# Optimization experiments

Measured on AMD Instinct MI355X. Metric: run time of the kernel, lower is better.

The kernel has to match this reference:

```python
import jax, jax.numpy as jnp
import numpy as np

B, T, D, H, L, V = 32, 128, 384, 6, 6, 32000
HS = D // H  # 64, head_size
EPS = 1e-5   # nn.LayerNorm default


def setup_inputs() -> dict:
    key = jax.random.key(0)
    ks = jax.random.split(key, 12)
    n = lambda k, shp: jax.random.normal(k, shp, dtype=jnp.float32) * 0.02
    return {
        'tokens': jax.random.randint(ks[0], (B, T), 0, V, dtype=jnp.int32),
        'tok_emb': n(ks[1], (V, D)),
        'pos_emb': n(ks[2], (T, D)),
        'Wq': n(ks[3], (L, H, D, HS)),
        'Wk': n(ks[4], (L, H, D, HS)),
        'Wv': n(ks[5], (L, H, D, HS)),
        'Wo': n(ks[6], (L, D, D)),
        'bo': jnp.zeros((L, D), jnp.float32),
        'W1': n(ks[7], (L, D, 4 * D)),
        'b1': jnp.zeros((L, 4 * D), jnp.float32),
        'W2': n(ks[8], (L, 4 * D, D)),
        'b2': jnp.zeros((L, D), jnp.float32),
        'g1': jnp.ones((L, D), jnp.float32),
        'be1': jnp.zeros((L, D), jnp.float32),
        'g2': jnp.ones((L, D), jnp.float32),
        'be2': jnp.zeros((L, D), jnp.float32),
        'gf': jnp.ones((D,), jnp.float32),
        'bef': jnp.zeros((D,), jnp.float32),
        'Wout': n(ks[9], (D, V)),
        'bout': jnp.zeros((V,), jnp.float32),
    }


def _ln(x, g, b):
    m = x.mean(-1, keepdims=True)
    v = ((x - m) ** 2).mean(-1, keepdims=True)
    return (x - m) * jax.lax.rsqrt(v + EPS) * g + b


def reference(tokens, tok_emb, pos_emb, Wq, Wk, Wv, Wo, bo, W1, b1, W2, b2,
              g1, be1, g2, be2, gf, bef, Wout, bout):
    t = tokens.shape[1]
    x = tok_emb[tokens] + pos_emb[:t]  # [B,T,D]
    mask = jnp.tril(jnp.ones((t, t), dtype=bool))
    scale = HS ** -0.5

    def block(x, p):
        wq, wk, wv, wo, bo_, w1, b1_, w2, b2_, g1_, be1_, g2_, be2_ = p
        h = _ln(x, g1_, be1_)
        q = jnp.einsum('btd,hde->bhte', h, wq)
        k = jnp.einsum('btd,hde->bhte', h, wk)
        v = jnp.einsum('btd,hde->bhte', h, wv)
        s = jnp.einsum('bhqe,bhke->bhqk', q, k) * scale
        s = jnp.where(mask, s, -jnp.inf)
        a = jax.nn.softmax(s, axis=-1)
        o = jnp.einsum('bhqk,bhke->bhqe', a, v)  # [B,H,T,HS]
        o = o.transpose(0, 2, 1, 3).reshape(x.shape[0], t, D)
        x = x + o @ wo + bo_
        h2 = _ln(x, g2_, be2_)
        x = x + jax.nn.relu(h2 @ w1 + b1_) @ w2 + b2_
        return x, None

    x, _ = jax.lax.scan(block, x, (Wq, Wk, Wv, Wo, bo, W1, b1, W2, b2,
                                   g1, be1, g2, be2))
    x = _ln(x, gf, bef)
    logits = x @ Wout + bout  # [B,T,V]
    return jax.nn.softmax(logits, axis=-1)
```

## Files before the change

kernel.cpp:

```cpp
#include <hip/hip_runtime.h>
#include <math.h>

#define NB 32
#define NT 128
#define ND 384
#define NH 6
#define NL 6
#define NV 32000
#define NHS 64
#define NBT (NB*NT)
#define NFF (4*ND)
#define NQKV (3*ND)
#define LNEPS 1e-5f

typedef unsigned short u16;
typedef unsigned int   u32;
typedef __attribute__((ext_vector_type(8))) short bf16x8;
typedef __attribute__((ext_vector_type(4))) float f32x4;

#define FLAG_BIAS 1
#define FLAG_RELU 2
#define FLAG_RESID 4
#define FLAG_BF16OUT 8

__device__ __forceinline__ float bf2f(u16 h) { return __uint_as_float((u32)h << 16); }
__device__ __forceinline__ u16 f2bf(float f) {
    u32 u = __float_as_uint(f);
    u32 r = u + 0x7fffu + ((u >> 16) & 1u);
    return (u16)(r >> 16);
}

__device__ __forceinline__ float wave_sum(float v) {
#pragma unroll
    for (int m = 1; m < 64; m <<= 1) v += __shfl_xor(v, m, 64);
    return v;
}
__device__ __forceinline__ float wave_max(float v) {
#pragma unroll
    for (int m = 1; m < 64; m <<= 1) v = fmaxf(v, __shfl_xor(v, m, 64));
    return v;
}

__global__ void embed_kernel(const int* __restrict__ tokens,
                             const float* __restrict__ te,
                             const float* __restrict__ pe,
                             float* __restrict__ x) {
    int i = blockIdx.x * 256 + threadIdx.x;
    if (i >= NBT * ND) return;
    int d  = i % ND;
    int bt = i / ND;
    int t  = bt % NT;
    int tok = tokens[bt];
    x[i] = te[(size_t)tok * ND + d] + pe[t * ND + d];
}

__global__ __launch_bounds__(256) void transpose_cvt_kernel(
    const float* __restrict__ in, u16* __restrict__ out,
    int R, int C, long in_z_stride, long out_z_stride, int zH, long out_h_stride)
{
    __shared__ float tile[32][33];
    int z = blockIdx.z;
    long in_off = (long)z * in_z_stride;
    long out_off;
    if (zH > 1) { int l = z / zH, h = z % zH;
        out_off = (long)l * out_z_stride + (long)h * out_h_stride; }
    else out_off = (long)z * out_z_stride;
    int r0 = blockIdx.y * 32, c0 = blockIdx.x * 32;
    int tx = threadIdx.x & 31, ty = threadIdx.x >> 5;
#pragma unroll
    for (int i = 0; i < 32; i += 8)
        tile[ty + i][tx] = in[in_off + (size_t)(r0 + ty + i) * C + c0 + tx];
    __syncthreads();
#pragma unroll
    for (int i = 0; i < 32; i += 8)
        out[out_off + (size_t)(c0 + ty + i) * R + r0 + tx] = f2bf(tile[tx][ty + i]);
}

template <int BF16OUT>
__global__ __launch_bounds__(256) void ln_kernel(const float* __restrict__ x,
                                                 const float* __restrict__ g,
                                                 const float* __restrict__ be,
                                                 float* __restrict__ outf,
                                                 u16* __restrict__ outb) {
    __shared__ float red[4];
    int row = blockIdx.x, tid = threadIdx.x;
    const float* xr = x + (size_t)row * ND;
    float v0 = xr[tid];
    bool has1 = (tid + 256) < ND;
    float v1 = has1 ? xr[tid + 256] : 0.f;

    float s = wave_sum(v0 + v1);
    if ((tid & 63) == 0) red[tid >> 6] = s;
    __syncthreads();
    float mean = (red[0] + red[1] + red[2] + red[3]) * (1.f / ND);
    __syncthreads();

    float d0 = v0 - mean;
    float d1 = has1 ? (v1 - mean) : 0.f;
    float ss = wave_sum(d0 * d0 + d1 * d1);
    if ((tid & 63) == 0) red[tid >> 6] = ss;
    __syncthreads();
    float rstd = rsqrtf((red[0] + red[1] + red[2] + red[3]) * (1.f / ND) + LNEPS);

    float o0 = d0 * rstd * g[tid] + be[tid];
    if (BF16OUT) {
        u16* orow = outb + (size_t)row * ND;
        orow[tid] = f2bf(o0);
        if (has1) orow[tid + 256] = f2bf(d1 * rstd * g[tid + 256] + be[tid + 256]);
    } else {
        float* orow = outf + (size_t)row * ND;
        orow[tid] = o0;
        if (has1) orow[tid + 256] = d1 * rstd * g[tid + 256] + be[tid + 256];
    }
}

#define BM 128
#define BN 128
#define BK 32
#define KPAD 40

__global__ __launch_bounds__(256) void gemm_bf16_kernel(
    const u16* __restrict__ A,
    const u16* __restrict__ Bt,
    const float* __restrict__ bias,
    float* __restrict__ Cf,
    u16* __restrict__ Cb,
    int M, int N, int K, int flags)
{
    __shared__ u16 As[BM * KPAD];
    __shared__ u16 Bs[BN * KPAD];
    int tid = threadIdx.x;
    int bn = blockIdx.x, bm = blockIdx.y;
    int row0 = bm * BM, col0 = bn * BN;
    int wave = tid >> 6, lane = tid & 63;
    int wr = wave >> 1, wc = wave & 1;
    int lrow = lane & 15;
    int kgrp = lane >> 4;

    f32x4 acc[4][4];
#pragma unroll
    for (int i = 0; i < 4; i++)
#pragma unroll
        for (int j = 0; j < 4; j++) acc[i][j] = (f32x4){0.f, 0.f, 0.f, 0.f};

    int c0 = tid * 2;
    int sr0 = c0 >> 2, sk0 = (c0 & 3) * 8;
    int c1 = c0 + 1;
    int sr1 = c1 >> 2, sk1 = (c1 & 3) * 8;

    const size_t arow0 = (size_t)(row0 + sr0) * K;
    const size_t arow1 = (size_t)(row0 + sr1) * K;
    const size_t brow0 = (size_t)(col0 + sr0) * K;
    const size_t brow1 = (size_t)(col0 + sr1) * K;

    for (int k0 = 0; k0 < K; k0 += BK) {
        bf16x8 a0 = *(const bf16x8*)&A[arow0 + k0 + sk0];
        bf16x8 a1 = *(const bf16x8*)&A[arow1 + k0 + sk1];
        bf16x8 b0 = *(const bf16x8*)&Bt[brow0 + k0 + sk0];
        bf16x8 b1 = *(const bf16x8*)&Bt[brow1 + k0 + sk1];
        __syncthreads();
        *(bf16x8*)&As[sr0 * KPAD + sk0] = a0;
        *(bf16x8*)&As[sr1 * KPAD + sk1] = a1;
        *(bf16x8*)&Bs[sr0 * KPAD + sk0] = b0;
        *(bf16x8*)&Bs[sr1 * KPAD + sk1] = b1;
        __syncthreads();

        bf16x8 af[4], bfr[4];
#pragma unroll
        for (int mi = 0; mi < 4; mi++)
            af[mi] = *(const bf16x8*)&As[(wr * 64 + mi * 16 + lrow) * KPAD + kgrp * 8];
#pragma unroll
        for (int ni = 0; ni < 4; ni++)
            bfr[ni] = *(const bf16x8*)&Bs[(wc * 64 + ni * 16 + lrow) * KPAD + kgrp * 8];
#pragma unroll
        for (int mi = 0; mi < 4; mi++)
#pragma unroll
            for (int ni = 0; ni < 4; ni++)
                acc[mi][ni] = __builtin_amdgcn_mfma_f32_16x16x32_bf16(
                    af[mi], bfr[ni], acc[mi][ni], 0, 0, 0);
    }

#pragma unroll
    for (int mi = 0; mi < 4; mi++) {
#pragma unroll
        for (int ni = 0; ni < 4; ni++) {
            int c = col0 + wc * 64 + ni * 16 + lrow;
            int rb = row0 + wr * 64 + mi * 16 + kgrp * 4;
#pragma unroll
            for (int j = 0; j < 4; j++) {
                size_t idx = (size_t)(rb + j) * N + c;
                float v = acc[mi][ni][j];
                if (flags & FLAG_BIAS) v += bias[c];
                if (flags & FLAG_RELU) v = fmaxf(v, 0.f);
                if (flags & FLAG_RESID) v += Cf[idx];
                if (flags & FLAG_BF16OUT) Cb[idx] = f2bf(v);
                else Cf[idx] = v;
            }
        }
    }
}

__global__ __launch_bounds__(256) void gemm_f32_kernel(const float* __restrict__ A,
                                                       const float* __restrict__ Bm,
                                                       const float* __restrict__ bias,
                                                       float* __restrict__ C,
                                                       int M, int N, int K, int flags) {
    __shared__ float Asl[16][65];
    __shared__ float Bsl[16][64];
    int bn = blockIdx.x, bm = blockIdx.y;
    int tid = threadIdx.x;
    int tr = tid >> 4, tc = tid & 15;
    int row0 = bm * 64, col0 = bn * 64;
    float acc[4][4];
#pragma unroll
    for (int i = 0; i < 4; i++)
#pragma unroll
        for (int j = 0; j < 4; j++) acc[i][j] = 0.f;

    for (int k0 = 0; k0 < K; k0 += 16) {
#pragma unroll
        for (int i = tid; i < 1024; i += 256) {
            int r = i >> 4, c = i & 15;
            Asl[c][r] = A[(size_t)(row0 + r) * K + (k0 + c)];
        }
#pragma unroll
        for (int i = tid; i < 1024; i += 256) {
            int r = i >> 6, c = i & 63;
            Bsl[r][c] = Bm[(size_t)(k0 + r) * N + (col0 + c)];
        }
        __syncthreads();
#pragma unroll
        for (int kk = 0; kk < 16; kk++) {
            float a[4], bv[4];
#pragma unroll
            for (int i = 0; i < 4; i++) a[i] = Asl[kk][tr * 4 + i];
#pragma unroll
            for (int j = 0; j < 4; j++) bv[j] = Bsl[kk][tc * 4 + j];
#pragma unroll
            for (int i = 0; i < 4; i++)
#pragma unroll
                for (int j = 0; j < 4; j++) acc[i][j] += a[i] * bv[j];
        }
        __syncthreads();
    }
#pragma unroll
    for (int i = 0; i < 4; i++) {
        size_t r = (size_t)row0 + tr * 4 + i;
#pragma unroll
        for (int j = 0; j < 4; j++) {
            int cc = col0 + tc * 4 + j;
            float t = acc[i][j];
            if (flags & 1) t += bias[cc];
            C[r * (size_t)N + cc] = t;
        }
    }
}

__global__ __launch_bounds__(128) void attn_kernel(const u16* __restrict__ qkv,
                                                   u16* __restrict__ o) {
    __shared__ float ks[NT][NHS];
    __shared__ float vs[NT][NHS];
    int bh = blockIdx.x;
    int b = bh / NH, h = bh % NH;
    int tid = threadIdx.x;
    size_t row0 = (size_t)b * NT;

    for (int i = tid; i < NT * (NHS / 8); i += 128) {
        int r = i >> 3, c8 = (i & 7) * 8;
        bf16x8 kv = *(const bf16x8*)&qkv[(row0 + r) * NQKV + ND + h * NHS + c8];
        bf16x8 vv = *(const bf16x8*)&qkv[(row0 + r) * NQKV + 2 * ND + h * NHS + c8];
#pragma unroll
        for (int j = 0; j < 8; j++) {
            ks[r][c8 + j] = bf2f((u16)kv[j]);
            vs[r][c8 + j] = bf2f((u16)vv[j]);
        }
    }
    float qr[NHS];
    {
        const u16* qp = &qkv[(row0 + tid) * NQKV + h * NHS];
#pragma unroll
        for (int e8 = 0; e8 < 8; e8++) {
            bf16x8 qv = *(const bf16x8*)(qp + e8 * 8);
#pragma unroll
            for (int j = 0; j < 8; j++) qr[e8 * 8 + j] = bf2f((u16)qv[j]);
        }
    }
    __syncthreads();

    const float scale = 0.125f;
    float m = -1e30f;
    for (int j = 0; j <= tid; ++j) {
        float dot = 0.f;
#pragma unroll
        for (int e = 0; e < NHS; e++) dot += qr[e] * ks[j][e];
        m = fmaxf(m, dot * scale);
    }
    float acc[NHS];
#pragma unroll
    for (int e = 0; e < NHS; e++) acc[e] = 0.f;
    float s = 0.f;
    for (int j = 0; j <= tid; ++j) {
        float dot = 0.f;
#pragma unroll
        for (int e = 0; e < NHS; e++) dot += qr[e] * ks[j][e];
        float p = __expf(dot * scale - m);
        s += p;
#pragma unroll
        for (int e = 0; e < NHS; e++) acc[e] += p * vs[j][e];
    }
    float inv = 1.f / s;
    u16* op = o + (row0 + tid) * ND + h * NHS;
#pragma unroll
    for (int e = 0; e < NHS; e++) op[e] = f2bf(acc[e] * inv);
}

__global__ __launch_bounds__(1024) void softmax_kernel(float* __restrict__ out) {
    __shared__ float red[16];
    int row = blockIdx.x, tid = threadIdx.x;
    float* p = out + (size_t)row * NV;
    const int nch = NV / 4;
    float4 v[8];
    float m = -1e30f;
#pragma unroll
    for (int i = 0; i < 8; i++) {
        int c = tid + i * 1024;
        if (c < nch) {
            v[i] = ((const float4*)p)[c];
            m = fmaxf(m, fmaxf(fmaxf(v[i].x, v[i].y), fmaxf(v[i].z, v[i].w)));
        }
    }
    m = wave_max(m);
    if ((tid & 63) == 0) red[tid >> 6] = m;
    __syncthreads();
    float mm = red[0];
#pragma unroll
    for (int i = 1; i < 16; i++) mm = fmaxf(mm, red[i]);
    __syncthreads();
    float s = 0.f;
#pragma unroll
    for (int i = 0; i < 8; i++) {
        int c = tid + i * 1024;
        if (c < nch) {
            v[i].x = __expf(v[i].x - mm); v[i].y = __expf(v[i].y - mm);
            v[i].z = __expf(v[i].z - mm); v[i].w = __expf(v[i].w - mm);
            s += v[i].x + v[i].y + v[i].z + v[i].w;
        }
    }
    s = wave_sum(s);
    if ((tid & 63) == 0) red[tid >> 6] = s;
    __syncthreads();
    float ss = 0.f;
#pragma unroll
    for (int i = 0; i < 16; i++) ss += red[i];
    float inv = 1.f / ss;
#pragma unroll
    for (int i = 0; i < 8; i++) {
        int c = tid + i * 1024;
        if (c < nch) {
            v[i].x *= inv; v[i].y *= inv; v[i].z *= inv; v[i].w *= inv;
            ((float4*)p)[c] = v[i];
        }
    }
}

extern "C" void kernel_launch(void* const* d_in, const int* in_sizes, int n_in,
                              void* d_out, int out_size, void* d_ws, size_t ws_size,
                              hipStream_t stream) {
    const int*   tokens  = (const int*)d_in[0];
    const float* tok_emb = (const float*)d_in[1];
    const float* pos_emb = (const float*)d_in[2];
    const float* Wq      = (const float*)d_in[3];
    const float* Wk      = (const float*)d_in[4];
    const float* Wv      = (const float*)d_in[5];
    const float* Wo      = (const float*)d_in[6];
    const float* bo      = (const float*)d_in[7];
    const float* W1      = (const float*)d_in[8];
    const float* b1      = (const float*)d_in[9];
    const float* W2      = (const float*)d_in[10];
    const float* b2      = (const float*)d_in[11];
    const float* g1      = (const float*)d_in[12];
    const float* be1     = (const float*)d_in[13];
    const float* g2      = (const float*)d_in[14];
    const float* be2     = (const float*)d_in[15];
    const float* gf      = (const float*)d_in[16];
    const float* bef     = (const float*)d_in[17];
    const float* Wout    = (const float*)d_in[18];
    const float* bout    = (const float*)d_in[19];
    float* out = (float*)d_out;

    const size_t S_hb   = (size_t)NBT * ND * 2;
    const size_t S_wout = (size_t)NV * ND * 2;
    const size_t S_x    = (size_t)NBT * ND * 4;
    const size_t S_qkv  = (size_t)NBT * NQKV * 2;
    const size_t S_o    = (size_t)NBT * ND * 2;
    const size_t S_u    = (size_t)NBT * NFF * 2;
    const size_t S_wqkv = (size_t)NL * NQKV * ND * 2;
    const size_t S_wo   = (size_t)NL * ND * ND * 2;
    const size_t S_w1   = (size_t)NL * ND * NFF * 2;
    const size_t S_w2   = (size_t)NL * NFF * ND * 2;
    const size_t S_hf   = (size_t)NBT * ND * 4;
    auto al = [](size_t x) { return (x + 255) & ~(size_t)255; };

    const size_t needA = al(S_hb) + al(S_wout) + al(S_x) + al(S_qkv) + al(S_o) +
                         al(S_u) + al(S_wqkv) + al(S_wo) + al(S_w1) + al(S_w2);
    const size_t needB = al(S_hb) + al(S_wout);

    char* wsb  = (char*)d_ws;
    char* outb = (char*)d_out;
    bool fp32_logits = false;

    u16 *hb, *woutt, *qkvb, *ob, *ub, *wqkvt, *wot, *w1t, *w2t;
    float *xbuf, *hf = nullptr;

    if (ws_size >= needA) {
        char* p = wsb;
        hb    = (u16*)p; p += al(S_hb);
        woutt = (u16*)p; p += al(S_wout);
        xbuf  = (float*)p; p += al(S_x);
        qkvb  = (u16*)p; p += al(S_qkv);
        ob    = (u16*)p; p += al(S_o);
        ub    = (u16*)p; p += al(S_u);
        wqkvt = (u16*)p; p += al(S_wqkv);
        wot   = (u16*)p; p += al(S_wo);
        w1t   = (u16*)p; p += al(S_w1);
        w2t   = (u16*)p; p += al(S_w2);
    } else if (ws_size >= needB) {
        char* p = wsb;
        hb    = (u16*)p; p += al(S_hb);
        woutt = (u16*)p; p += al(S_wout);
        char* q = outb;
        xbuf  = (float*)q; q += al(S_x);
        qkvb  = (u16*)q; q += al(S_qkv);
        ob    = (u16*)q; q += al(S_o);
        ub    = (u16*)q; q += al(S_u);
        wqkvt = (u16*)q; q += al(S_wqkv);
        wot   = (u16*)q; q += al(S_wo);
        w1t   = (u16*)q; q += al(S_w1);
        w2t   = (u16*)q; q += al(S_w2);
    } else {
        fp32_logits = true;
        hf = (float*)wsb;
        woutt = nullptr;
        char* q = outb;
        hb    = (u16*)q; q += al(S_hb);
        xbuf  = (float*)q; q += al(S_x);
        qkvb  = (u16*)q; q += al(S_qkv);
        ob    = (u16*)q; q += al(S_o);
        ub    = (u16*)q; q += al(S_u);
        wqkvt = (u16*)q; q += al(S_wqkv);
        wot   = (u16*)q; q += al(S_wo);
        w1t   = (u16*)q; q += al(S_w1);
        w2t   = (u16*)q; q += al(S_w2);
    }

    {
        const float* Wsides[3] = {Wq, Wk, Wv};
        for (int s = 0; s < 3; s++)
            transpose_cvt_kernel<<<dim3(NHS / 32, ND / 32, NL * NH), 256, 0, stream>>>(
                Wsides[s], wqkvt + (size_t)s * ND * ND, ND, NHS,
                (long)ND * NHS, (long)NQKV * ND, NH, (long)NHS * ND);
        transpose_cvt_kernel<<<dim3(ND / 32, ND / 32, NL), 256, 0, stream>>>(
            Wo, wot, ND, ND, (long)ND * ND, (long)ND * ND, 1, 0);
        transpose_cvt_kernel<<<dim3(NFF / 32, ND / 32, NL), 256, 0, stream>>>(
            W1, w1t, ND, NFF, (long)ND * NFF, (long)NFF * ND, 1, 0);
        transpose_cvt_kernel<<<dim3(ND / 32, NFF / 32, NL), 256, 0, stream>>>(
            W2, w2t, NFF, ND, (long)NFF * ND, (long)ND * NFF, 1, 0);
        if (!fp32_logits)
            transpose_cvt_kernel<<<dim3(NV / 32, ND / 32, 1), 256, 0, stream>>>(
                Wout, woutt, ND, NV, 0, 0, 1, 0);
    }

    int n = NBT * ND;
    embed_kernel<<<(n + 255) / 256, 256, 0, stream>>>(tokens, tok_emb, pos_emb, xbuf);

    dim3 g_qkv(NQKV / BN, NBT / BM);
    dim3 g_d(ND / BN, NBT / BM);
    dim3 g_ff(NFF / BN, NBT / BM);
    dim3 g_out(NV / BN, NBT / BM);

    for (int l = 0; l < NL; l++) {
        ln_kernel<1><<<NBT, 256, 0, stream>>>(xbuf, g1 + l * ND, be1 + l * ND, nullptr, hb);
        gemm_bf16_kernel<<<g_qkv, 256, 0, stream>>>(hb, wqkvt + (size_t)l * NQKV * ND,
            nullptr, nullptr, qkvb, NBT, NQKV, ND, FLAG_BF16OUT);
        attn_kernel<<<NB * NH, 128, 0, stream>>>(qkvb, ob);
        gemm_bf16_kernel<<<g_d, 256, 0, stream>>>(ob, wot + (size_t)l * ND * ND,
            bo + l * ND, xbuf, nullptr, NBT, ND, ND, FLAG_BIAS | FLAG_RESID);
        ln_kernel<1><<<NBT, 256, 0, stream>>>(xbuf, g2 + l * ND, be2 + l * ND, nullptr, hb);
        gemm_bf16_kernel<<<g_ff, 256, 0, stream>>>(hb, w1t + (size_t)l * ND * NFF,
            b1 + l * NFF, nullptr, ub, NBT, NFF, ND, FLAG_BIAS | FLAG_RELU | FLAG_BF16OUT);
        gemm_bf16_kernel<<<g_d, 256, 0, stream>>>(ub, w2t + (size_t)l * NFF * ND,
            b2 + l * ND, xbuf, nullptr, NBT, ND, NFF, FLAG_BIAS | FLAG_RESID);
    }

    if (!fp32_logits) {
        ln_kernel<1><<<NBT, 256, 0, stream>>>(xbuf, gf, bef, nullptr, hb);
        gemm_bf16_kernel<<<g_out, 256, 0, stream>>>(hb, woutt, bout, out, nullptr,
            NBT, NV, ND, FLAG_BIAS);
    } else {
        ln_kernel<0><<<NBT, 256, 0, stream>>>(xbuf, gf, bef, hf, nullptr);
        gemm_f32_kernel<<<dim3(NV / 64, NBT / 64), 256, 0, stream>>>(
            hf, Wout, bout, out, NBT, NV, ND, 1);
    }
    softmax_kernel<<<NBT, 1024, 0, stream>>>(out);
}
```

Measured before the change: 2.731 ms.

## Fuse transformer layers into persistent megakernel with grid barriers

Replaces the per-layer sequence of LN, GEMM and attention launches with one persistent kernel that loops over layers, separated by atomic-counter grid barriers. It also merges embedding and all weight transposes into a single prep launch, switches LayerNorm to one wave per row, and widens attention blocks to 256 threads with half of them idle. The goal is to remove launch overhead and inter-kernel gaps across about 40 small launches. The risks are barrier cost, low per-phase parallelism (few tiles for 512 blocks), and deadlock if blocks are not co-resident, which a spin timeout guards.

```diff
diff --git a/kernel.cpp b/kernel.cpp
--- a/kernel.cpp
+++ b/kernel.cpp
@@ -41,76 +41,34 @@
     return v;
 }
 
-__global__ void embed_kernel(const int* __restrict__ tokens,
-                             const float* __restrict__ te,
-                             const float* __restrict__ pe,
-                             float* __restrict__ x) {
-    int i = blockIdx.x * 256 + threadIdx.x;
-    if (i >= NBT * ND) return;
-    int d  = i % ND;
-    int bt = i / ND;
-    int t  = bt % NT;
-    int tok = tokens[bt];
-    x[i] = te[(size_t)tok * ND + d] + pe[t * ND + d];
-}
-
-__global__ __launch_bounds__(256) void transpose_cvt_kernel(
-    const float* __restrict__ in, u16* __restrict__ out,
-    int R, int C, long in_z_stride, long out_z_stride, int zH, long out_h_stride)
-{
-    __shared__ float tile[32][33];
-    int z = blockIdx.z;
-    long in_off = (long)z * in_z_stride;
-    long out_off;
-    if (zH > 1) { int l = z / zH, h = z % zH;
-        out_off = (long)l * out_z_stride + (long)h * out_h_stride; }
-    else out_off = (long)z * out_z_stride;
-    int r0 = blockIdx.y * 32, c0 = blockIdx.x * 32;
-    int tx = threadIdx.x & 31, ty = threadIdx.x >> 5;
-#pragma unroll
-    for (int i = 0; i < 32; i += 8)
-        tile[ty + i][tx] = in[in_off + (size_t)(r0 + ty + i) * C + c0 + tx];
-    __syncthreads();
-#pragma unroll
-    for (int i = 0; i < 32; i += 8)
-        out[out_off + (size_t)(c0 + ty + i) * R + r0 + tx] = f2bf(tile[tx][ty + i]);
-}
 
 template <int BF16OUT>
-__global__ __launch_bounds__(256) void ln_kernel(const float* __restrict__ x,
-                                                 const float* __restrict__ g,
-                                                 const float* __restrict__ be,
-                                                 float* __restrict__ outf,
-                                                 u16* __restrict__ outb) {
-    __shared__ float red[4];
-    int row = blockIdx.x, tid = threadIdx.x;
+__device__ __forceinline__ void dev_ln_rows(const float* __restrict__ x,
+        const float* __restrict__ g, const float* __restrict__ be,
+        float* __restrict__ outf, u16* __restrict__ outb, int row) {
+    int lane = threadIdx.x & 63;
     const float* xr = x + (size_t)row * ND;
-    float v0 = xr[tid];
-    bool has1 = (tid + 256) < ND;
-    float v1 = has1 ? xr[tid + 256] : 0.f;
-
-    float s = wave_sum(v0 + v1);
-    if ((tid & 63) == 0) red[tid >> 6] = s;
-    __syncthreads();
-    float mean = (red[0] + red[1] + red[2] + red[3]) * (1.f / ND);
-    __syncthreads();
-
-    float d0 = v0 - mean;
-    float d1 = has1 ? (v1 - mean) : 0.f;
-    float ss = wave_sum(d0 * d0 + d1 * d1);
-    if ((tid & 63) == 0) red[tid >> 6] = ss;
-    __syncthreads();
-    float rstd = rsqrtf((red[0] + red[1] + red[2] + red[3]) * (1.f / ND) + LNEPS);
-
-    float o0 = d0 * rstd * g[tid] + be[tid];
+    float v[6];
+    float s = 0.f;
+#pragma unroll
+    for (int i = 0; i < 6; i++) { v[i] = xr[lane * 6 + i]; s += v[i]; }
+    s = wave_sum(s);
+    float mean = s * (1.f / ND);
+    float ss = 0.f;
+#pragma unroll
+    for (int i = 0; i < 6; i++) { v[i] -= mean; ss += v[i] * v[i]; }
+    ss = wave_sum(ss);
+    float rstd = rsqrtf(ss * (1.f / ND) + LNEPS);
     if (BF16OUT) {
         u16* orow = outb + (size_t)row * ND;
-        orow[tid] = f2bf(o0);
-        if (has1) orow[tid + 256] = f2bf(d1 * rstd * g[tid + 256] + be[tid + 256]);
+#pragma unroll
+        for (int i = 0; i < 6; i++)
+            orow[lane * 6 + i] = f2bf(v[i] * rstd * g[lane * 6 + i] + be[lane * 6 + i]);
     } else {
         float* orow = outf + (size_t)row * ND;
-        orow[tid] = o0;
-        if (has1) orow[tid + 256] = d1 * rstd * g[tid + 256] + be[tid + 256];
+#pragma unroll
+        for (int i = 0; i < 6; i++)
+            orow[lane * 6 + i] = v[i] * rstd * g[lane * 6 + i] + be[lane * 6 + i];
     }
 }
 
@@ -119,18 +77,12 @@
 #define BK 32
 #define KPAD 40
 
-__global__ __launch_bounds__(256) void gemm_bf16_kernel(
-    const u16* __restrict__ A,
-    const u16* __restrict__ Bt,
-    const float* __restrict__ bias,
-    float* __restrict__ Cf,
-    u16* __restrict__ Cb,
-    int M, int N, int K, int flags)
+__device__ __forceinline__ void dev_gemm_tile(
+    const u16* __restrict__ A, const u16* __restrict__ Bt,
+    const float* __restrict__ bias, float* __restrict__ Cf, u16* __restrict__ Cb,
+    int N, int K, int bm, int bn, int flags, u16* As, u16* Bs)
 {
-    __shared__ u16 As[BM * KPAD];
-    __shared__ u16 Bs[BN * KPAD];
     int tid = threadIdx.x;
-    int bn = blockIdx.x, bm = blockIdx.y;
     int row0 = bm * BM, col0 = bn * BN;
     int wave = tid >> 6, lane = tid & 63;
     int wr = wave >> 1, wc = wave & 1;
@@ -147,7 +99,6 @@
     int sr0 = c0 >> 2, sk0 = (c0 & 3) * 8;
     int c1 = c0 + 1;
     int sr1 = c1 >> 2, sk1 = (c1 & 3) * 8;
-
     const size_t arow0 = (size_t)(row0 + sr0) * K;
     const size_t arow1 = (size_t)(row0 + sr1) * K;
     const size_t brow0 = (size_t)(col0 + sr0) * K;
@@ -179,7 +130,6 @@
                 acc[mi][ni] = __builtin_amdgcn_mfma_f32_16x16x32_bf16(
                     af[mi], bfr[ni], acc[mi][ni], 0, 0, 0);
     }
-
 #pragma unroll
     for (int mi = 0; mi < 4; mi++) {
 #pragma unroll
@@ -200,11 +150,127 @@
     }
 }
 
+__device__ __forceinline__ void dev_attn(const u16* __restrict__ qkv,
+                                         u16* __restrict__ o, int bh,
+                                         float* ks, float* vs) {
+    __syncthreads();
+    int b = bh / NH, h = bh % NH;
+    int tid = threadIdx.x;
+    size_t row0 = (size_t)b * NT;
+
+    for (int i = tid; i < NT * (NHS / 8); i += 256) {
+        int r = i >> 3, c8 = (i & 7) * 8;
+        bf16x8 kv = *(const bf16x8*)&qkv[(row0 + r) * NQKV + ND + h * NHS + c8];
+        bf16x8 vv = *(const bf16x8*)&qkv[(row0 + r) * NQKV + 2 * ND + h * NHS + c8];
+#pragma unroll
+        for (int j = 0; j < 8; j++) {
+            ks[r * NHS + c8 + j] = bf2f((u16)kv[j]);
+            vs[r * NHS + c8 + j] = bf2f((u16)vv[j]);
+        }
+    }
+    float qr[NHS];
+    if (tid < NT) {
+        const u16* qp = &qkv[(row0 + tid) * NQKV + h * NHS];
+#pragma unroll
+        for (int e8 = 0; e8 < 8; e8++) {
+            bf16x8 qv = *(const bf16x8*)(qp + e8 * 8);
+#pragma unroll
+            for (int j = 0; j < 8; j++) qr[e8 * 8 + j] = bf2f((u16)qv[j]);
+        }
+    }
+    __syncthreads();
+    if (tid < NT) {
+        const float scale = 0.125f;
+        float m = -1e30f;
+        for (int j = 0; j <= tid; ++j) {
+            float dot = 0.f;
+#pragma unroll
+            for (int e = 0; e < NHS; e++) dot += qr[e] * ks[j * NHS + e];
+            m = fmaxf(m, dot * scale);
+        }
+        float acc[NHS];
+#pragma unroll
+        for (int e = 0; e < NHS; e++) acc[e] = 0.f;
+        float s = 0.f;
+        for (int j = 0; j <= tid; ++j) {
+            float dot = 0.f;
+#pragma unroll
+            for (int e = 0; e < NHS; e++) dot += qr[e] * ks[j * NHS + e];
+            float p = __expf(dot * scale - m);
+            s += p;
+#pragma unroll
+            for (int e = 0; e < NHS; e++) acc[e] += p * vs[j * NHS + e];
+        }
+        float inv = 1.f / s;
+        u16* op = o + (row0 + tid) * ND + h * NHS;
+#pragma unroll
+        for (int e = 0; e < NHS; e++) op[e] = f2bf(acc[e] * inv);
+    }
+}
+
+__device__ __forceinline__ void dev_transpose(const float* __restrict__ in,
+        u16* __restrict__ out, int R, int C, long izs, long ozs, int zH, long ohs,
+        int z, int r0, int c0, float (*tile)[33]) {
+    long in_off = (long)z * izs;
+    long out_off;
+    if (zH > 1) { int l = z / zH, h = z % zH; out_off = (long)l * ozs + (long)h * ohs; }
+    else out_off = (long)z * ozs;
+    int tx = threadIdx.x & 31, ty = threadIdx.x >> 5;
+#pragma unroll
+    for (int i = 0; i < 32; i += 8)
+        tile[ty + i][tx] = in[in_off + (size_t)(r0 + ty + i) * C + c0 + tx];
+    __syncthreads();
+#pragma unroll
+    for (int i = 0; i < 32; i += 8)
+        out[out_off + (size_t)(c0 + ty + i) * R + r0 + tx] = f2bf(tile[tx][ty + i]);
+}
+
+
+__global__ void embed_kernel(const int* __restrict__ tokens,
+                             const float* __restrict__ te,
+                             const float* __restrict__ pe,
+                             float* __restrict__ x) {
+    int i = blockIdx.x * 256 + threadIdx.x;
+    if (i >= NBT * ND) return;
+    int d = i % ND, bt = i / ND, t = bt % NT;
+    x[i] = te[(size_t)tokens[bt] * ND + d] + pe[t * ND + d];
+}
+
+__global__ __launch_bounds__(256) void transpose_cvt_kernel(
+    const float* __restrict__ in, u16* __restrict__ out,
+    int R, int C, long izs, long ozs, int zH, long ohs) {
+    __shared__ float tile[32][33];
+    dev_transpose(in, out, R, C, izs, ozs, zH, ohs,
+                  blockIdx.z, blockIdx.y * 32, blockIdx.x * 32, tile);
+}
+
+template <int BF16OUT>
+__global__ __launch_bounds__(256) void ln_kernel(const float* __restrict__ x,
+        const float* __restrict__ g, const float* __restrict__ be,
+        float* __restrict__ outf, u16* __restrict__ outb) {
+    int r = blockIdx.x * 4 + (threadIdx.x >> 6);
+    dev_ln_rows<BF16OUT>(x, g, be, outf, outb, r);
+}
+
+__global__ __launch_bounds__(256) void gemm_bf16_kernel(
+    const u16* __restrict__ A, const u16* __restrict__ Bt,
+    const float* __restrict__ bias, float* __restrict__ Cf, u16* __restrict__ Cb,
+    int N, int K, int flags) {
+    __shared__ u16 As[BM * KPAD];
+    __shared__ u16 Bs[BN * KPAD];
+    dev_gemm_tile(A, Bt, bias, Cf, Cb, N, K, blockIdx.y, blockIdx.x, flags, As, Bs);
+}
+
+__global__ __launch_bounds__(256) void attn_kernel(const u16* __restrict__ qkv,
+                                                   u16* __restrict__ o) {
+    __shared__ float ks[NT * NHS];
+    __shared__ float vs[NT * NHS];
+    dev_attn(qkv, o, blockIdx.x, ks, vs);
+}
+
 __global__ __launch_bounds__(256) void gemm_f32_kernel(const float* __restrict__ A,
-                                                       const float* __restrict__ Bm,
-                                                       const float* __restrict__ bias,
-                                                       float* __restrict__ C,
-                                                       int M, int N, int K, int flags) {
+        const float* __restrict__ Bm, const float* __restrict__ bias,
+        float* __restrict__ C, int M, int N, int K, int flags) {
     __shared__ float Asl[16][65];
     __shared__ float Bsl[16][64];
     int bn = blockIdx.x, bm = blockIdx.y;
@@ -216,7 +282,6 @@
     for (int i = 0; i < 4; i++)
 #pragma unroll
         for (int j = 0; j < 4; j++) acc[i][j] = 0.f;
-
     for (int k0 = 0; k0 < K; k0 += 16) {
 #pragma unroll
         for (int i = tid; i < 1024; i += 256) {
@@ -254,64 +319,6 @@
             C[r * (size_t)N + cc] = t;
         }
     }
-}
-
-__global__ __launch_bounds__(128) void attn_kernel(const u16* __restrict__ qkv,
-                                                   u16* __restrict__ o) {
-    __shared__ float ks[NT][NHS];
-    __shared__ float vs[NT][NHS];
-    int bh = blockIdx.x;
-    int b = bh / NH, h = bh % NH;
-    int tid = threadIdx.x;
-    size_t row0 = (size_t)b * NT;
-
-    for (int i = tid; i < NT * (NHS / 8); i += 128) {
-        int r = i >> 3, c8 = (i & 7) * 8;
-        bf16x8 kv = *(const bf16x8*)&qkv[(row0 + r) * NQKV + ND + h * NHS + c8];
-        bf16x8 vv = *(const bf16x8*)&qkv[(row0 + r) * NQKV + 2 * ND + h * NHS + c8];
-#pragma unroll
-        for (int j = 0; j < 8; j++) {
-            ks[r][c8 + j] = bf2f((u16)kv[j]);
-            vs[r][c8 + j] = bf2f((u16)vv[j]);
-        }
-    }
-    float qr[NHS];
-    {
-        const u16* qp = &qkv[(row0 + tid) * NQKV + h * NHS];
-#pragma unroll
-        for (int e8 = 0; e8 < 8; e8++) {
-            bf16x8 qv = *(const bf16x8*)(qp + e8 * 8);
-#pragma unroll
-            for (int j = 0; j < 8; j++) qr[e8 * 8 + j] = bf2f((u16)qv[j]);
-        }
-    }
-    __syncthreads();
-
-    const float scale = 0.125f;
-    float m = -1e30f;
-    for (int j = 0; j <= tid; ++j) {
-        float dot = 0.f;
-#pragma unroll
-        for (int e = 0; e < NHS; e++) dot += qr[e] * ks[j][e];
-        m = fmaxf(m, dot * scale);
-    }
-    float acc[NHS];
-#pragma unroll
-    for (int e = 0; e < NHS; e++) acc[e] = 0.f;
-    float s = 0.f;
-    for (int j = 0; j <= tid; ++j) {
-        float dot = 0.f;
-#pragma unroll
-        for (int e = 0; e < NHS; e++) dot += qr[e] * ks[j][e];
-        float p = __expf(dot * scale - m);
-        s += p;
-#pragma unroll
-        for (int e = 0; e < NHS; e++) acc[e] += p * vs[j][e];
-    }
-    float inv = 1.f / s;
-    u16* op = o + (row0 + tid) * ND + h * NHS;
-#pragma unroll
-    for (int e = 0; e < NHS; e++) op[e] = f2bf(acc[e] * inv);
 }
 
 __global__ __launch_bounds__(1024) void softmax_kernel(float* __restrict__ out) {
@@ -362,6 +369,133 @@
         }
     }
 }
+
+
+#define PREP_GRID 28512
+
+__global__ __launch_bounds__(256) void prep_kernel(
+    const int* __restrict__ tokens, const float* __restrict__ te,
+    const float* __restrict__ pe, float* __restrict__ xbuf,
+    const float* __restrict__ Wq, const float* __restrict__ Wk,
+    const float* __restrict__ Wv, const float* __restrict__ Wo,
+    const float* __restrict__ W1, const float* __restrict__ W2,
+    const float* __restrict__ Wout,
+    u16* __restrict__ wqkvt, u16* __restrict__ wot, u16* __restrict__ w1t,
+    u16* __restrict__ w2t, u16* __restrict__ woutt)
+{
+    __shared__ float tile[32][33];
+    int bid = blockIdx.x, tid = threadIdx.x;
+    const int nE = (NBT * ND) / 256;
+    const int nQ = NL * NH * (ND / 32) * (NHS / 32);
+    const int nWo = NL * (ND / 32) * (ND / 32);
+    const int nW1 = NL * (ND / 32) * (NFF / 32);
+    const int nW2 = NL * (NFF / 32) * (ND / 32);
+    const int s0 = nE, s3 = s0 + 3 * nQ, s4 = s3 + nWo, s5 = s4 + nW1, s6 = s5 + nW2;
+
+    if (bid < s0) {
+        int i = bid * 256 + tid;
+        int d = i % ND, bt = i / ND, t = bt % NT;
+        xbuf[i] = te[(size_t)tokens[bt] * ND + d] + pe[t * ND + d];
+        return;
+    }
+    const float* in; u16* out; int R, C, zH; long izs, ozs, ohs; int local;
+    if (bid < s3) {
+        int w = (bid - s0) / nQ;
+        local = (bid - s0) % nQ;
+        in = (w == 0) ? Wq : (w == 1) ? Wk : Wv;
+        out = wqkvt + (size_t)w * ND * ND;
+        R = ND; C = NHS; izs = (long)ND * NHS; ozs = (long)NQKV * ND; zH = NH; ohs = (long)NHS * ND;
+    } else if (bid < s4) {
+        local = bid - s3; in = Wo; out = wot;
+        R = ND; C = ND; izs = (long)ND * ND; ozs = (long)ND * ND; zH = 1; ohs = 0;
+    } else if (bid < s5) {
+        local = bid - s4; in = W1; out = w1t;
+        R = ND; C = NFF; izs = (long)ND * NFF; ozs = (long)NFF * ND; zH = 1; ohs = 0;
+    } else if (bid < s6) {
+        local = bid - s5; in = W2; out = w2t;
+        R = NFF; C = ND; izs = (long)NFF * ND; ozs = (long)ND * NFF; zH = 1; ohs = 0;
+    } else {
+        local = bid - s6; in = Wout; out = woutt;
+        R = ND; C = NV; izs = 0; ozs = 0; zH = 1; ohs = 0;
+    }
+    int tC = C / 32, tR = R / 32, perz = tR * tC;
+    int z = local / perz, rem = local % perz;
+    int rt = rem / tC, ct = rem % tC;
+    dev_transpose(in, out, R, C, izs, ozs, zH, ohs, z, rt * 32, ct * 32, tile);
+}
+
+
+__device__ __forceinline__ void gsync(unsigned* bar, unsigned gen_target, int nblk) {
+    __syncthreads();
+    if (threadIdx.x == 0) {
+        __threadfence();
+        if (atomicAdd(&bar[0], 1u) == (unsigned)nblk - 1u) {
+            atomicExch(&bar[0], 0u);
+            __threadfence();
+            atomicAdd(&bar[1], 1u);
+        } else {
+            long spin = 0;
+            while (atomicAdd(&bar[1], 0u) < gen_target) {
+                __builtin_amdgcn_s_sleep(8);
+                if (++spin > 10000000L) break;
+            }
+        }
+    }
+    __syncthreads();
+    __threadfence();
+}
+
+__global__ __launch_bounds__(256, 2) void mega_kernel(
+    float* __restrict__ xbuf, u16* __restrict__ hb, u16* __restrict__ qkvb,
+    u16* __restrict__ ob, u16* __restrict__ ub,
+    const u16* __restrict__ wqkvt, const u16* __restrict__ wot,
+    const u16* __restrict__ w1t, const u16* __restrict__ w2t,
+    const float* __restrict__ g1, const float* __restrict__ be1,
+    const float* __restrict__ g2, const float* __restrict__ be2,
+    const float* __restrict__ gf, const float* __restrict__ bef,
+    const float* __restrict__ bo, const float* __restrict__ b1,
+    const float* __restrict__ b2, unsigned* bar, int nblk)
+{
+    __shared__ char smem[65536];
+    u16* As = (u16*)smem;
+    u16* Bs = (u16*)(smem + BM * KPAD * 2);
+    float* ks = (float*)smem;
+    float* vs = (float*)(smem + NT * NHS * 4);
+    int wid = threadIdx.x >> 6;
+    unsigned g = 0;
+
+    for (int l = 0; l < NL; l++) {
+        for (int r = blockIdx.x * 4 + wid; r < NBT; r += nblk * 4)
+            dev_ln_rows<1>(xbuf, g1 + l * ND, be1 + l * ND, nullptr, hb, r);
+        gsync(bar, ++g, nblk);
+        for (int t = blockIdx.x; t < (NQKV / BN) * (NBT / BM); t += nblk)
+            dev_gemm_tile(hb, wqkvt + (size_t)l * NQKV * ND, nullptr, nullptr, qkvb,
+                          NQKV, ND, t / (NQKV / BN), t % (NQKV / BN), FLAG_BF16OUT, As, Bs);
+        gsync(bar, ++g, nblk);
+        for (int t = blockIdx.x; t < NB * NH; t += nblk)
+            dev_attn(qkvb, ob, t, ks, vs);
+        gsync(bar, ++g, nblk);
+        for (int t = blockIdx.x; t < (ND / BN) * (NBT / BM); t += nblk)
+            dev_gemm_tile(ob, wot + (size_t)l * ND * ND, bo + l * ND, xbuf, nullptr,
+                          ND, ND, t / (ND / BN), t % (ND / BN), FLAG_BIAS | FLAG_RESID, As, Bs);
+        gsync(bar, ++g, nblk);
+        for (int r = blockIdx.x * 4 + wid; r < NBT; r += nblk * 4)
+            dev_ln_rows<1>(xbuf, g2 + l * ND, be2 + l * ND, nullptr, hb, r);
+        gsync(bar, ++g, nblk);
+        for (int t = blockIdx.x; t < (NFF / BN) * (NBT / BM); t += nblk)
+            dev_gemm_tile(hb, w1t + (size_t)l * ND * NFF, b1 + l * NFF, nullptr, ub,
+                          NFF, ND, t / (NFF / BN), t % (NFF / BN),
+                          FLAG_BIAS | FLAG_RELU | FLAG_BF16OUT, As, Bs);
+        gsync(bar, ++g, nblk);
+        for (int t = blockIdx.x; t < (ND / BN) * (NBT / BM); t += nblk)
+            dev_gemm_tile(ub, w2t + (size_t)l * NFF * ND, b2 + l * ND, xbuf, nullptr,
+                          ND, NFF, t / (ND / BN), t % (ND / BN), FLAG_BIAS | FLAG_RESID, As, Bs);
+        gsync(bar, ++g, nblk);
+    }
+    for (int r = blockIdx.x * 4 + wid; r < NBT; r += nblk * 4)
+        dev_ln_rows<1>(xbuf, gf, bef, nullptr, hb, r);
+}
+
 
 extern "C" void kernel_launch(void* const* d_in, const int* in_sizes, int n_in,
                               void* d_out, int out_size, void* d_ws, size_t ws_size,
@@ -398,12 +532,11 @@
     const size_t S_wo   = (size_t)NL * ND * ND * 2;
     const size_t S_w1   = (size_t)NL * ND * NFF * 2;
     const size_t S_w2   = (size_t)NL * NFF * ND * 2;
-    const size_t S_hf   = (size_t)NBT * ND * 4;
     auto al = [](size_t x) { return (x + 255) & ~(size_t)255; };
 
     const size_t needA = al(S_hb) + al(S_wout) + al(S_x) + al(S_qkv) + al(S_o) +
-                         al(S_u) + al(S_wqkv) + al(S_wo) + al(S_w1) + al(S_w2);
-    const size_t needB = al(S_hb) + al(S_wout);
+                         al(S_u) + al(S_wqkv) + al(S_wo) + al(S_w1) + al(S_w2) + 256;
+    const size_t needB = al(S_hb) + al(S_wout) + 256;
 
     char* wsb  = (char*)d_ws;
     char* outb = (char*)d_out;
@@ -411,6 +544,7 @@
 
     u16 *hb, *woutt, *qkvb, *ob, *ub, *wqkvt, *wot, *w1t, *w2t;
     float *xbuf, *hf = nullptr;
+    unsigned* bar = nullptr;
 
     if (ws_size >= needA) {
         char* p = wsb;
@@ -424,10 +558,12 @@
         wot   = (u16*)p; p += al(S_wo);
         w1t   = (u16*)p; p += al(S_w1);
         w2t   = (u16*)p; p += al(S_w2);
+        bar   = (unsigned*)p;
     } else if (ws_size >= needB) {
         char* p = wsb;
         hb    = (u16*)p; p += al(S_hb);
         woutt = (u16*)p; p += al(S_wout);
+        bar   = (unsigned*)p;
         char* q = outb;
         xbuf  = (float*)q; q += al(S_x);
         qkvb  = (u16*)q; q += al(S_qkv);
@@ -453,7 +589,20 @@
         w2t   = (u16*)q; q += al(S_w2);
     }
 
-    {
+    int occ = 0;
+    hipOccupancyMaxActiveBlocksPerMultiprocessor(&occ, mega_kernel, 256, 0);
+    int nblk = (occ >= 2) ? 512 : (occ == 1 ? 256 : 0);
+    bool use_mega = (!fp32_logits) && (nblk > 0) && (bar != nullptr);
+
+    if (use_mega) {
+        prep_kernel<<<PREP_GRID, 256, 0, stream>>>(
+            tokens, tok_emb, pos_emb, xbuf, Wq, Wk, Wv, Wo, W1, W2, Wout,
+            wqkvt, wot, w1t, w2t, woutt);
+        hipMemsetAsync(bar, 0, 64, stream);
+        mega_kernel<<<nblk, 256, 0, stream>>>(
+            xbuf, hb, qkvb, ob, ub, wqkvt, wot, w1t, w2t,
+            g1, be1, g2, be2, gf, bef, bo, b1, b2, bar, nblk);
+    } else {
         const float* Wsides[3] = {Wq, Wk, Wv};
         for (int s = 0; s < 3; s++)
             transpose_cvt_kernel<<<dim3(NHS / 32, ND / 32, NL * NH), 256, 0, stream>>>(
@@ -468,36 +617,35 @@
         if (!fp32_logits)
             transpose_cvt_kernel<<<dim3(NV / 32, ND / 32, 1), 256, 0, stream>>>(
                 Wout, woutt, ND, NV, 0, 0, 1, 0);
-    }
-
-    int n = NBT * ND;
-    embed_kernel<<<(n + 255) / 256, 256, 0, stream>>>(tokens, tok_emb, pos_emb, xbuf);
-
-    dim3 g_qkv(NQKV / BN, NBT / BM);
-    dim3 g_d(ND / BN, NBT / BM);
-    dim3 g_ff(NFF / BN, NBT / BM);
-    dim3 g_out(NV / BN, NBT / BM);
-
-    for (int l = 0; l < NL; l++) {
-        ln_kernel<1><<<NBT, 256, 0, stream>>>(xbuf, g1 + l * ND, be1 + l * ND, nullptr, hb);
-        gemm_bf16_kernel<<<g_qkv, 256, 0, stream>>>(hb, wqkvt + (size_t)l * NQKV * ND,
-            nullptr, nullptr, qkvb, NBT, NQKV, ND, FLAG_BF16OUT);
-        attn_kernel<<<NB * NH, 128, 0, stream>>>(qkvb, ob);
-        gemm_bf16_kernel<<<g_d, 256, 0, stream>>>(ob, wot + (size_t)l * ND * ND,
-            bo + l * ND, xbuf, nullptr, NBT, ND, ND, FLAG_BIAS | FLAG_RESID);
-        ln_kernel<1><<<NBT, 256, 0, stream>>>(xbuf, g2 + l * ND, be2 + l * ND, nullptr, hb);
-        gemm_bf16_kernel<<<g_ff, 256, 0, stream>>>(hb, w1t + (size_t)l * ND * NFF,
-            b1 + l * NFF, nullptr, ub, NBT, NFF, ND, FLAG_BIAS | FLAG_RELU | FLAG_BF16OUT);
-        gemm_bf16_kernel<<<g_d, 256, 0, stream>>>(ub, w2t + (size_t)l * NFF * ND,
-            b2 + l * ND, xbuf, nullptr, NBT, ND, NFF, FLAG_BIAS | FLAG_RESID);
+        int n = NBT * ND;
+        embed_kernel<<<(n + 255) / 256, 256, 0, stream>>>(tokens, tok_emb, pos_emb, xbuf);
+
+        dim3 g_qkv(NQKV / BN, NBT / BM);
+        dim3 g_d(ND / BN, NBT / BM);
+        dim3 g_ff(NFF / BN, NBT / BM);
+        for (int l = 0; l < NL; l++) {
+            ln_kernel<1><<<NBT / 4, 256, 0, stream>>>(xbuf, g1 + l * ND, be1 + l * ND, nullptr, hb);
+            gemm_bf16_kernel<<<g_qkv, 256, 0, stream>>>(hb, wqkvt + (size_t)l * NQKV * ND,
+                nullptr, nullptr, qkvb, NQKV, ND, FLAG_BF16OUT);
+            attn_kernel<<<NB * NH, 256, 0, stream>>>(qkvb, ob);
+            gemm_bf16_kernel<<<g_d, 256, 0, stream>>>(ob, wot + (size_t)l * ND * ND,
+                bo + l * ND, xbuf, nullptr, ND, ND, FLAG_BIAS | FLAG_RESID);
+            ln_kernel<1><<<NBT / 4, 256, 0, stream>>>(xbuf, g2 + l * ND, be2 + l * ND, nullptr, hb);
+            gemm_bf16_kernel<<<g_ff, 256, 0, stream>>>(hb, w1t + (size_t)l * ND * NFF,
+                b1 + l * NFF, nullptr, ub, NFF, ND, FLAG_BIAS | FLAG_RELU | FLAG_BF16OUT);
+            gemm_bf16_kernel<<<g_d, 256, 0, stream>>>(ub, w2t + (size_t)l * NFF * ND,
+                b2 + l * ND, xbuf, nullptr, ND, NFF, FLAG_BIAS | FLAG_RESID);
+        }
+        if (!fp32_logits)
+            ln_kernel<1><<<NBT / 4, 256, 0, stream>>>(xbuf, gf, bef, nullptr, hb);
+        else
+            ln_kernel<0><<<NBT / 4, 256, 0, stream>>>(xbuf, gf, bef, hf, nullptr);
     }
 
     if (!fp32_logits) {
-        ln_kernel<1><<<NBT, 256, 0, stream>>>(xbuf, gf, bef, nullptr, hb);
-        gemm_bf16_kernel<<<g_out, 256, 0, stream>>>(hb, woutt, bout, out, nullptr,
-            NBT, NV, ND, FLAG_BIAS);
+        gemm_bf16_kernel<<<dim3(NV / BN, NBT / BM), 256, 0, stream>>>(
+            hb, woutt, bout, out, nullptr, NV, ND, FLAG_BIAS);
     } else {
-        ln_kernel<0><<<NBT, 256, 0, stream>>>(xbuf, gf, bef, hf, nullptr);
         gemm_f32_kernel<<<dim3(NV / 64, NBT / 64), 256, 0, stream>>>(
             hf, Wout, bout, out, NBT, NV, ND, 1);
     }
```

Result: slower. 4.029 ms (+47.5%).
